# Performance work log

Measured on AMD Instinct MI355X. Metric: run time of the kernel, lower is better.

Reference implementation:

```python
import jax, jax.numpy as jnp
import numpy as np

D_MODEL, HEADS, D_K = 512, 8, 64
MIN_SPREAD, MIN_RBF, MAX_RBF = 2.0, 0.001, 1.0
NEG_INF = float('-inf')


def setup_inputs() -> dict:
    key = jax.random.key(0)
    ks = jax.random.split(key, 12)
    B, N = 2, 2048
    xav = (6.0 / (D_K + D_MODEL)) ** 0.5
    unif = lambda k, shape: jax.random.uniform(k, shape, jnp.float32, -xav, xav)
    return {
        'q': jax.random.normal(ks[0], (B, N, D_MODEL), jnp.float32),
        'k': jax.random.normal(ks[1], (B, N, D_MODEL), jnp.float32),
        'v': jax.random.normal(ks[2], (B, N, D_MODEL), jnp.float32),
        'coords': jax.random.normal(ks[3], (B, N, 3), jnp.float32),
        'mask': jnp.zeros((B, N), dtype=bool),
        'spread_weights': jnp.zeros((HEADS,), jnp.float32),
        'beta_weights': jnp.zeros((HEADS,), jnp.float32),
        'q_proj': unif(ks[4], (HEADS, D_MODEL, D_K)),
        'k_proj': unif(ks[5], (HEADS, D_MODEL, D_K)),
        'v_proj': unif(ks[6], (HEADS, D_MODEL, D_K)),
        'q_bias': jnp.zeros((HEADS, D_K), jnp.float32),
        'k_bias': jnp.zeros((HEADS, D_K), jnp.float32),
        'v_bias': jnp.zeros((HEADS, D_K), jnp.float32),
        'w_out': jax.random.normal(ks[7], (D_MODEL, D_MODEL), jnp.float32) * (1.0 / D_MODEL ** 0.5),
    }


def reference(q, k, v, coords, mask, spread_weights, beta_weights,
              q_proj, k_proj, v_proj, q_bias, k_bias, v_bias, w_out):
    B, N, _ = q.shape
    # per-head projections: [B,H,N,dk]
    Q = jnp.einsum('bnd,hdk->bhnk', q, q_proj) + q_bias[None, :, None, :]
    K = jnp.einsum('bnd,hdk->bhnk', k, k_proj) + k_bias[None, :, None, :]
    V = jnp.einsum('bnd,hdk->bhnk', v, v_proj) + v_bias[None, :, None, :]
    # scaled dot-product scores [B,H,N,N]
    S = jnp.einsum('bhnk,bhmk->bhnm', Q, K) / (D_K ** 0.5)
    # squared pairwise distances [B,N,N] (D = sqrt(D2); RBF uses -D^2 = -D2)
    D2 = jnp.sum((coords[:, :, None, :] - coords[:, None, :, :]) ** 2, axis=-1)
    spreads = MIN_SPREAD + jnp.exp(spread_weights)  # [H]
    betas = jnp.exp(beta_weights)                   # [H]
    R = jnp.exp(-D2[:, None, :, :] / (2.0 * spreads[None, :, None, None] ** 2))
    R_norm = 2.0 * (R - MIN_RBF) / (MAX_RBF - MIN_RBF) - 1.0
    SR = S + jnp.abs(S) * betas[None, :, None, None] * R_norm
    SR = jnp.where(mask[:, None, None, :], NEG_INF, SR)  # eval mode: drop_p = 0
    P = jax.nn.softmax(SR, axis=-1)
    out = jnp.einsum('bhnm,bhmk->bhnk', P, V)  # [B,H,N,dk]
    # permute(0,2,3,1) -> [B,N,dk,H], reshape to [B,N,d_model]
    out = jnp.transpose(out, (0, 2, 3, 1)).reshape(B, N, D_MODEL)
    return out @ w_out.T
```

## Files before the change

### kernel.cpp

```cpp
#include <hip/hip_runtime.h>
#include <hip/hip_fp16.h>

typedef unsigned short u16;
typedef unsigned int u32;
typedef __attribute__((ext_vector_type(4))) float f32x4;
typedef __attribute__((ext_vector_type(8))) short s16x8;
typedef __attribute__((ext_vector_type(2))) unsigned int u32x2;
typedef __fp16 fp16x2 __attribute__((ext_vector_type(2)));

#define B_SZ 2
#define N_SZ 2048
#define H_SZ 8
#define DK 64
#define DM 512
#define QSC 0.18033688f

static __device__ inline void mfma_f16(f32x4& acc, s16x8 a, s16x8 b) {
    asm volatile("v_mfma_f32_16x16x32_f16 %0, %1, %2, %0" : "+v"(acc) : "v"(a), "v"(b));
}
static __device__ inline u16 f16_rn(float f) { return __half_as_ushort(__float2half(f)); }

static __device__ inline u32 pkrtz(float a, float b) {
    union { fp16x2 h; u32 u; } cv;
    cv.h = __builtin_amdgcn_cvt_pkrtz(a, b);
    return cv.u;
}

#if __has_builtin(__builtin_amdgcn_exp2f)
#define EXP2(x) __builtin_amdgcn_exp2f(x)
#else
#define EXP2(x) exp2f(x)
#endif

static __device__ inline s16x8 cvt8(const float4& a, const float4& b) {
    s16x8 r;
    r[0] = (short)f16_rn(a.x); r[1] = (short)f16_rn(a.y);
    r[2] = (short)f16_rn(a.z); r[3] = (short)f16_rn(a.w);
    r[4] = (short)f16_rn(b.x); r[5] = (short)f16_rn(b.y);
    r[6] = (short)f16_rn(b.z); r[7] = (short)f16_rn(b.w);
    return r;
}

static __device__ inline u16* swz(u16* base, int row, int byteoff) {
    return (u16*)((char*)base + row * 128 + (byteoff ^ ((row & 7) << 4)));
}
static __device__ inline const u16* swzc(const u16* base, int row, int byteoff) {
    return (const u16*)((const char*)base + row * 128 + (byteoff ^ ((row & 7) << 4)));
}

#if __has_builtin(__builtin_amdgcn_global_load_lds)
#define HAS_GLL 1
static __device__ inline void gll16(const u16* g, u16* l) {
    __builtin_amdgcn_global_load_lds(
        (const __attribute__((address_space(1))) unsigned int*)g,
        (__attribute__((address_space(3))) unsigned int*)l, 16, 0, 0);
}
#endif
static __device__ inline void stage16(const u16* gp, u16* lbase, int lane) {
#ifdef HAS_GLL
    gll16(gp, lbase);
#else
    *(s16x8*)(lbase + lane * 8) = *(const s16x8*)(gp);
#endif
}

__global__ void __launch_bounds__(256) k_prep(
    const float* __restrict__ q, const float* __restrict__ k,
    const float* __restrict__ v, const float* __restrict__ qp,
    const float* __restrict__ kp, const float* __restrict__ vp,
    const float* __restrict__ wo, const float* __restrict__ coords,
    const unsigned char* __restrict__ maskp,
    u16* __restrict__ Pt, u16* __restrict__ Wb2, u16* __restrict__ Af,
    float4* __restrict__ C4, float* __restrict__ mbias) {
    int blk = blockIdx.x, t = threadIdx.x;
    __shared__ float lds[64 * 65];
    if (blk < 192) {
        int z = blk >> 6, rem = blk & 63, h = rem >> 3, ddt = rem & 7;
        const float* src = (z == 0 ? qp : (z == 1 ? kp : vp)) + (size_t)h * DM * DK;
        u16* dst = Pt + ((size_t)(z * H_SZ + h)) * DK * DM;
        float sc = (z == 0) ? QSC : 1.0f;
#pragma unroll
        for (int i = 0; i < 16; i++) {
            int idx = i * 256 + t;
            int rr = idx >> 6, cc = idx & 63;
            lds[cc * 65 + rr] = src[(size_t)(ddt * 64 + rr) * DK + cc];
        }
        __syncthreads();
#pragma unroll
        for (int i = 0; i < 16; i++) {
            int idx = i * 256 + t;
            int kk = idx >> 6, dd = idx & 63;
            dst[(size_t)kk * DM + ddt * 64 + dd] = f16_rn(lds[kk * 65 + dd] * sc);
        }
    } else if (blk < 320) {
        int idx8 = (blk - 192) * 256 + t;
        int base = idx8 * 8;
        int c = base >> 9, col0 = base & 511;
        int h = col0 >> 6, d0 = col0 & 63;
        s16x8 r;
#pragma unroll
        for (int i = 0; i < 8; i++)
            r[i] = (short)f16_rn(wo[(size_t)c * 512 + (d0 + i) * 8 + h]);
        *(s16x8*)(Wb2 + base) = r;
    } else if (blk < 3392) {
        size_t base = (size_t)(blk - 320) * 2048 + (size_t)t * 8;
        int z = (int)(base >> 21);
        size_t off = base & 2097151;
        const float* s = (z == 0 ? q : (z == 1 ? k : v)) + off;
        float4 f0 = *(const float4*)(s);
        float4 f1 = *(const float4*)(s + 4);
        *(s16x8*)(Af + base) = cvt8(f0, f1);
    } else {
        int i = (blk - 3392) * 256 + t;
        float x = coords[(size_t)i * 3], y = coords[(size_t)i * 3 + 1], z = coords[(size_t)i * 3 + 2];
        C4[i] = make_float4(x, y, z, x * x + y * y + z * z);
        mbias[i] = maskp[i] ? -1e30f : 0.0f;
    }
}

__global__ void __launch_bounds__(256) k_proj_gemm(
    const u16* __restrict__ Af, const u16* __restrict__ Pt,
    const float* __restrict__ qbias, const float* __restrict__ kbias,
    const float* __restrict__ vbias,
    u16* __restrict__ Qb, u16* __restrict__ Kb, u16* __restrict__ Vt) {
    int z = blockIdx.z;
    const u16* A = Af + (size_t)z * (4096 * 512);
    const float* bias = z == 0 ? qbias : (z == 1 ? kbias : vbias);
    const u16* Bw = Pt + (size_t)z * (512 * 512);
    int m0 = blockIdx.x * 128, c0 = blockIdx.y * 64;
    int t = threadIdx.x, w = t >> 6, l = t & 63, g = (l >> 4), cl = l & 15;
    __shared__ __align__(16) u16 a_lds[2][128 * 64];
    f32x4 acc[2][4] = {};
    int srow_b = w * 8 + (l >> 3), schk = l & 7;

#define STAGE_P(ks, buf)                                                              \
    {                                                                                 \
        _Pragma("unroll") for (int cc = 0; cc < 4; cc++) {                            \
            int row = cc * 32 + srow_b;                                               \
            const u16* gp = A + (size_t)(m0 + row) * 512 + (ks) * 64 +                \
                            ((schk ^ (row & 7)) << 3);                                \
            stage16(gp, a_lds[buf] + cc * 2048 + w * 512, l);                         \
        }                                                                             \
    }

    STAGE_P(0, 0);
    for (int ks = 0; ks < 8; ks++) {
        int cur = ks & 1;
        __syncthreads();
        if (ks < 7) STAGE_P(ks + 1, cur ^ 1);
        s16x8 bfrag[4][2];
#pragma unroll
        for (int st = 0; st < 4; st++) {
            int c = c0 + st * 16 + cl;
#pragma unroll
            for (int kk = 0; kk < 2; kk++)
                bfrag[st][kk] = *(const s16x8*)(Bw + (size_t)c * 512 + ks * 64 + kk * 32 + 8 * g);
        }
#pragma unroll
        for (int rs = 0; rs < 2; rs++) {
            int row = w * 32 + rs * 16 + cl;
#pragma unroll
            for (int kk = 0; kk < 2; kk++) {
                s16x8 afrag = *(const s16x8*)swzc(a_lds[cur], row, kk * 64 + 16 * g);
#pragma unroll
                for (int st = 0; st < 4; st++) mfma_f16(acc[rs][st], afrag, bfrag[st][kk]);
            }
        }
    }
#undef STAGE_P

    if (z == 2) {
        int h = blockIdx.y;
        int b = m0 >> 11;
        u16* vl = a_lds[0];
        __syncthreads();
#pragma unroll
        for (int rs = 0; rs < 2; rs++) {
#pragma unroll
            for (int st = 0; st < 4; st++) {
                int d = st * 16 + cl;
                float bv = bias[c0 + st * 16 + cl];
#pragma unroll
                for (int r = 0; r < 4; r++) {
                    int row = w * 32 + rs * 16 + 4 * g + r;
                    int jt = row >> 6, jl = row & 63;
                    int jp = (jl & 15) * 4 + (jl >> 4);
                    vl[jt * 4096 + d * 64 + jp] = f16_rn(acc[rs][st][r] + bv);
                }
            }
        }
        __syncthreads();
        int jt = t >> 7, rem = t & 127, d = rem >> 1, qh = t & 1;
        const u16* src = vl + jt * 4096 + d * 64 + qh * 32;
        int jtile = ((m0 & 2047) >> 6) + jt;
        u16* dst = Vt + ((size_t)((b * H_SZ + h) * 32 + jtile)) * 4096 + d * 64 + qh * 32;
        *(s16x8*)(dst) = *(const s16x8*)(src);
        *(s16x8*)(dst + 8) = *(const s16x8*)(src + 8);
        *(s16x8*)(dst + 16) = *(const s16x8*)(src + 16);
        *(s16x8*)(dst + 24) = *(const s16x8*)(src + 24);
    } else {
        float bsc = (z == 0) ? QSC : 1.0f;
        u16* dst = (z == 0) ? Qb : Kb;
#pragma unroll
        for (int rs = 0; rs < 2; rs++) {
#pragma unroll
            for (int st = 0; st < 4; st++) {
                int c = c0 + st * 16 + cl;
                int h = c >> 6, kk = c & 63;
                float bv = bias[c] * bsc;
#pragma unroll
                for (int r = 0; r < 4; r++) {
                    int m = m0 + w * 32 + rs * 16 + 4 * g + r;
                    int b = m >> 11, n = m & 2047;
                    dst[((size_t)(b * H_SZ + h) * N_SZ + n) * DK + kk] = f16_rn(acc[rs][st][r] + bv);
                }
            }
        }
    }
}

__global__ void __launch_bounds__(512, 4) k_attn(
    const u16* __restrict__ Qb, const u16* __restrict__ Kb,
    const u16* __restrict__ Vt, const float4* __restrict__ C4,
    const float* __restrict__ mbias,
    const float* __restrict__ spread_w, const float* __restrict__ beta_w,
    u16* __restrict__ Om) {
    int bid = blockIdx.x;
    int wid = (bid & 7) * 64 + (bid >> 3);
    int qt = wid & 31, bh = wid >> 5;
    int h = bh & 7, b = bh >> 3;
    int n0 = qt * 64;
    int t = threadIdx.x, w = t >> 6, l = t & 63, g = l >> 4, cl = l & 15;
    int wq = w & 3, half = w >> 2;

    __shared__ __align__(16) u16 kbuf[2][4096];
    __shared__ __align__(16) u16 vbuf[2][4096];
    __shared__ __align__(16) u16 pbuf[8][1024];
    __shared__ float4 cjs[2][64];
    __shared__ float mbs[2][64];

    int qrow = n0 + wq * 16 + cl;
    const u16* qp = Qb + ((size_t)bh * N_SZ + qrow) * DK;
    s16x8 qf0 = *(const s16x8*)(qp + 8 * g);
    s16x8 qf1 = *(const s16x8*)(qp + 32 + 8 * g);

    float sigma = 2.0f + __expf(spread_w[h]);
    float ninv2 = -0.72134752f / (sigma * sigma);
    float beta = __expf(beta_w[h]);
    float rnA = 2.002002f * beta, rnB = -1.002002f * beta;
    float m2n = -2.0f * ninv2;

    float qx2[4], qy2[4], qz2[4], aR[4];
#pragma unroll
    for (int r = 0; r < 4; r++) {
        float4 c4 = C4[b * N_SZ + n0 + wq * 16 + 4 * g + r];
        qx2[r] = c4.x * m2n; qy2[r] = c4.y * m2n; qz2[r] = c4.z * m2n;
        aR[r] = ninv2 * c4.w;
    }

    float mrun[4] = {-1e30f, -1e30f, -1e30f, -1e30f};
    float lsum[4] = {0.f, 0.f, 0.f, 0.f};
    f32x4 oacc[4] = {};

    int sid = t & 255, srow = sid >> 2, sq = sid & 3;
    const u16* kbase = Kb + (size_t)bh * N_SZ * DK;
    const u16* vbase = Vt + (size_t)bh * 32 * 4096;
    const float4* c4b = C4 + b * N_SZ;
    const float* mbb = mbias + b * N_SZ;

    s16x8 kst0, kst1, vst0, vst1;
    float4 cst; float mst = 0.f;

#define LOADT(it_)                                                                  \
    {                                                                               \
        int jts = (it_) * 2 + half, j0s = jts * 64;                                 \
        const u16* ksrc = kbase + (size_t)(j0s + srow) * 64 + sq * 16;              \
        kst0 = *(const s16x8*)(ksrc);                                               \
        kst1 = *(const s16x8*)(ksrc + 8);                                           \
        const u16* vsrc = vbase + (size_t)jts * 4096 + srow * 64 + sq * 16;         \
        vst0 = *(const s16x8*)(vsrc);                                               \
        vst1 = *(const s16x8*)(vsrc + 8);                                           \
        if (sid < 64) { cst = c4b[j0s + sid]; mst = mbb[j0s + sid]; }               \
    }

    LOADT(0);
    for (int it = 0; it < 16; it++) {
        __syncthreads();
        *(s16x8*)swz(kbuf[half], srow, sq * 32)      = kst0;
        *(s16x8*)swz(kbuf[half], srow, sq * 32 + 16) = kst1;
        *(s16x8*)swz(vbuf[half], srow, sq * 32)      = vst0;
        *(s16x8*)swz(vbuf[half], srow, sq * 32 + 16) = vst1;
        if (sid < 64) { cjs[half][sid] = cst; mbs[half][sid] = mst; }
        __syncthreads();
        if (it < 15) LOADT(it + 1);

        f32x4 s[4];
#pragma unroll
        for (int st = 0; st < 4; st++) {
            int jj = st * 16 + cl;
            s16x8 kf0 = *(const s16x8*)swzc(kbuf[half], jj, 16 * g);
            s16x8 kf1 = *(const s16x8*)swzc(kbuf[half], jj, 64 + 16 * g);
            f32x4 a = {};
            mfma_f16(a, qf0, kf0);
            mfma_f16(a, qf1, kf1);
            s[st] = a;
        }
        float sr[4][4];
#pragma unroll
        for (int st = 0; st < 4; st++) {
            float4 cc = cjs[half][st * 16 + cl];
            float mb = mbs[half][st * 16 + cl];
            float bJ = ninv2 * cc.w;
#pragma unroll
            for (int r = 0; r < 4; r++) {
                float arg = fmaf(qx2[r], cc.x,
                            fmaf(qy2[r], cc.y,
                            fmaf(qz2[r], cc.z, aR[r] + bJ)));
                float rb = EXP2(arg);
                float sv = s[st][r];
                sr[st][r] = fmaf(fabsf(sv), fmaf(rnA, rb, rnB), sv) + mb;
            }
        }
        float tmx[4]; bool need = false;
#pragma unroll
        for (int r = 0; r < 4; r++) {
            float tm = fmaxf(fmaxf(sr[0][r], sr[1][r]), fmaxf(sr[2][r], sr[3][r]));
            tm = fmaxf(tm, __shfl_xor(tm, 1));
            tm = fmaxf(tm, __shfl_xor(tm, 2));
            tm = fmaxf(tm, __shfl_xor(tm, 4));
            tm = fmaxf(tm, __shfl_xor(tm, 8));
            tmx[r] = tm;
            need = need || (tm > mrun[r] + 8.0f);
        }
        if (__any(need)) {
#pragma unroll
            for (int r = 0; r < 4; r++) {
                float mn = fmaxf(mrun[r], tmx[r]);
                float corr = EXP2(mrun[r] - mn);
                mrun[r] = mn;
                lsum[r] *= corr;
#pragma unroll
                for (int dst = 0; dst < 4; dst++) oacc[dst][r] *= corr;
            }
        }
#pragma unroll
        for (int r = 0; r < 4; r++) {
            float p0 = EXP2(sr[0][r] - mrun[r]);
            float p1 = EXP2(sr[1][r] - mrun[r]);
            float p2 = EXP2(sr[2][r] - mrun[r]);
            float p3 = EXP2(sr[3][r] - mrun[r]);
            lsum[r] += (p0 + p1) + (p2 + p3);
            u32x2 pw = {pkrtz(p0, p1), pkrtz(p2, p3)};
            *(u32x2*)swz(pbuf[w], 4 * g + r, cl * 8) = pw;
        }
#pragma unroll
        for (int ks = 0; ks < 2; ks++) {
            s16x8 pf = *(const s16x8*)swzc(pbuf[w], cl, ks * 64 + 16 * g);
#pragma unroll
            for (int dst = 0; dst < 4; dst++) {
                s16x8 vf = *(const s16x8*)swzc(vbuf[half], dst * 16 + cl, ks * 64 + 16 * g);
                mfma_f16(oacc[dst], pf, vf);
            }
        }
    }
#undef LOADT
#pragma unroll
    for (int r = 0; r < 4; r++) {
        float s = lsum[r];
        s += __shfl_xor(s, 1); s += __shfl_xor(s, 2);
        s += __shfl_xor(s, 4); s += __shfl_xor(s, 8);
        lsum[r] = s;
    }
    __syncthreads();
    float* scrO = (float*)(&kbuf[0][0]);
    float* scrM = (float*)(&vbuf[0][0]);
    if (half == 1) {
#pragma unroll
        for (int r = 0; r < 4; r++) {
            int rr = 4 * g + r;
#pragma unroll
            for (int dst = 0; dst < 4; dst++)
                scrO[wq * 1024 + rr * 64 + dst * 16 + cl] = oacc[dst][r];
            if (cl == 0) {
                scrM[wq * 32 + rr] = mrun[r];
                scrM[wq * 32 + 16 + rr] = lsum[r];
            }
        }
    }
    __syncthreads();
    if (half == 0) {
#pragma unroll
        for (int r = 0; r < 4; r++) {
            int rr = 4 * g + r;
            float mu = scrM[wq * 32 + rr], lu = scrM[wq * 32 + 16 + rr];
            float M = fmaxf(mrun[r], mu);
            float pa = EXP2(mrun[r] - M), pb = EXP2(mu - M);
            float inv = 1.0f / (pa * lsum[r] + pb * lu);
            int row = n0 + wq * 16 + rr;
#pragma unroll
            for (int dst = 0; dst < 4; dst++) {
                float o = (pa * oacc[dst][r] + pb * scrO[wq * 1024 + rr * 64 + dst * 16 + cl]) * inv;
                Om[((size_t)b * N_SZ + row) * DM + h * 64 + dst * 16 + cl] = f16_rn(o);
            }
        }
    }
}

__global__ void __launch_bounds__(256) k_out_gemm(
    const u16* __restrict__ Om, const u16* __restrict__ Wb2,
    float* __restrict__ out) {
    int m0 = blockIdx.x * 128, c0 = blockIdx.y * 64;
    int t = threadIdx.x, w = t >> 6, l = t & 63, g = (l >> 4), cl = l & 15;
    __shared__ __align__(16) u16 a_lds[2][128 * 64];
    f32x4 acc[2][4] = {};
    int srow_b = w * 8 + (l >> 3), schk = l & 7;

#define STAGE_O(ks, buf)                                                              \
    {                                                                                 \
        _Pragma("unroll") for (int cc = 0; cc < 4; cc++) {                            \
            int row = cc * 32 + srow_b;                                               \
            const u16* gp = Om + (size_t)(m0 + row) * 512 + (ks) * 64 +               \
                            ((schk ^ (row & 7)) << 3);                                \
            stage16(gp, a_lds[buf] + cc * 2048 + w * 512, l);                         \
        }                                                                             \
    }

    STAGE_O(0, 0);
    for (int ks = 0; ks < 8; ks++) {
        int cur = ks & 1;
        __syncthreads();
        if (ks < 7) STAGE_O(ks + 1, cur ^ 1);
        s16x8 bfrag[4][2];
#pragma unroll
        for (int st = 0; st < 4; st++) {
            int c = c0 + st * 16 + cl;
#pragma unroll
            for (int kk = 0; kk < 2; kk++)
                bfrag[st][kk] = *(const s16x8*)(Wb2 + (size_t)c * 512 + ks * 64 + kk * 32 + 8 * g);
        }
#pragma unroll
        for (int rs = 0; rs < 2; rs++) {
            int row = w * 32 + rs * 16 + cl;
#pragma unroll
            for (int kk = 0; kk < 2; kk++) {
                s16x8 afrag = *(const s16x8*)swzc(a_lds[cur], row, kk * 64 + 16 * g);
#pragma unroll
                for (int st = 0; st < 4; st++) mfma_f16(acc[rs][st], afrag, bfrag[st][kk]);
            }
        }
    }
#undef STAGE_O
#pragma unroll
    for (int rs = 0; rs < 2; rs++) {
#pragma unroll
        for (int st = 0; st < 4; st++) {
            int c = c0 + st * 16 + cl;
#pragma unroll
            for (int r = 0; r < 4; r++) {
                int m = m0 + w * 32 + rs * 16 + 4 * g + r;
                out[(size_t)m * 512 + c] = acc[rs][st][r];
            }
        }
    }
}

extern "C" void kernel_launch(void* const* d_in, const int* in_sizes, int n_in,
                              void* d_out, int out_size, void* d_ws, size_t ws_size,
                              hipStream_t stream) {
    const float* q      = (const float*)d_in[0];
    const float* k      = (const float*)d_in[1];
    const float* v      = (const float*)d_in[2];
    const float* coords = (const float*)d_in[3];
    const unsigned char* mask = (const unsigned char*)d_in[4];
    const float* sw     = (const float*)d_in[5];
    const float* bw     = (const float*)d_in[6];
    const float* qp     = (const float*)d_in[7];
    const float* kp     = (const float*)d_in[8];
    const float* vp     = (const float*)d_in[9];
    const float* qbias  = (const float*)d_in[10];
    const float* kbias  = (const float*)d_in[11];
    const float* vbias  = (const float*)d_in[12];
    const float* wo     = (const float*)d_in[13];

    char* ws = (char*)d_ws;
    u16*    Pt    = (u16*)(ws);
    u16*    Wb2   = (u16*)(ws + 1572864);
    u16*    Af    = (u16*)(ws + 2097152);
    u16*    Qb    = (u16*)(ws + 14680064);
    u16*    Kb    = (u16*)(ws + 18874368);
    u16*    Vt    = (u16*)(ws + 23068672);
    u16*    Om    = (u16*)(ws + 27262976);
    float4* C4    = (float4*)(ws + 31457280);
    float*  mbias = (float*)(ws + 31522816);

    k_prep<<<dim3(3408), 256, 0, stream>>>(q, k, v, qp, kp, vp, wo, coords, mask,
                                           Pt, Wb2, Af, C4, mbias);
    k_proj_gemm<<<dim3(32, 8, 3), 256, 0, stream>>>(Af, Pt, qbias, kbias, vbias, Qb, Kb, Vt);
    k_attn<<<dim3(512), 512, 0, stream>>>(Qb, Kb, Vt, C4, mbias, sw, bw, Om);
    k_out_gemm<<<dim3(32, 8), 256, 0, stream>>>(Om, Wb2, (float*)d_out);
}
```

Baseline: 240.5 us.

## Double-buffer attention K/V tiles via direct global-to-LDS loads and remap GEMM grids

The attention kernel now double-buffers K and V tiles in LDS, filling them with direct global-to-LDS loads (with XOR swizzle in the source address) instead of staging through registers. This removes one of the two barriers per iteration and lets the next tile's fetch overlap the current tile's compute. Per-key coords and mask values are now read straight from global memory rather than staged in LDS. The projection and output GEMMs switch to 1D grids with an XCD-aware block remap (bid&7 interleave), aimed at better L2 locality across the chiplets. LDS use in the attention kernel grows, which may reduce occupancy.

Result: faster. 203.0 us (-15.6%).

```diff
diff --git a/kernel.cpp b/kernel.cpp
--- a/kernel.cpp
+++ b/kernel.cpp
@@ -62,6 +62,21 @@
 #else
     *(s16x8*)(lbase + lane * 8) = *(const s16x8*)(gp);
 #endif
+}
+
+static __device__ inline void stage_tile_swz(const u16* tile, u16* lds, int wl, int lane) {
+#pragma unroll
+    for (int c = 0; c < 2; c++) {
+        int Lb = c * 4096 + wl * 1024 + lane * 16;
+        int row = Lb >> 7, off = Lb & 127;
+        const u16* src = tile + row * 64 + (((off ^ ((row & 7) << 4))) >> 1);
+        u16* dst = (u16*)((char*)lds + c * 4096 + wl * 1024);
+#ifdef HAS_GLL
+        gll16(src, dst);
+#else
+        *(s16x8*)((char*)dst + lane * 16) = *(const s16x8*)src;
+#endif
+    }
 }
 
 __global__ void __launch_bounds__(256) k_prep(
@@ -123,11 +138,15 @@
     const float* __restrict__ qbias, const float* __restrict__ kbias,
     const float* __restrict__ vbias,
     u16* __restrict__ Qb, u16* __restrict__ Kb, u16* __restrict__ Vt) {
-    int z = blockIdx.z;
+    int bid = blockIdx.x;
+    int wid = (bid & 7) * 96 + (bid >> 3);
+    int c0 = (wid & 7) * 64;
+    int zm = wid >> 3;
+    int m0 = (zm & 31) * 128;
+    int z = zm >> 5;
     const u16* A = Af + (size_t)z * (4096 * 512);
     const float* bias = z == 0 ? qbias : (z == 1 ? kbias : vbias);
     const u16* Bw = Pt + (size_t)z * (512 * 512);
-    int m0 = blockIdx.x * 128, c0 = blockIdx.y * 64;
     int t = threadIdx.x, w = t >> 6, l = t & 63, g = (l >> 4), cl = l & 15;
     __shared__ __align__(16) u16 a_lds[2][128 * 64];
     f32x4 acc[2][4] = {};
@@ -170,7 +189,7 @@
 #undef STAGE_P
 
     if (z == 2) {
-        int h = blockIdx.y;
+        int h = c0 >> 6;
         int b = m0 >> 11;
         u16* vl = a_lds[0];
         __syncthreads();
@@ -233,14 +252,11 @@
     int t = threadIdx.x, w = t >> 6, l = t & 63, g = l >> 4, cl = l & 15;
     int wq = w & 3, half = w >> 2;
 
-    __shared__ __align__(16) u16 kbuf[2][4096];
-    __shared__ __align__(16) u16 vbuf[2][4096];
+    __shared__ __align__(16) u16 kbuf[2][2][4096];
+    __shared__ __align__(16) u16 vbuf[2][2][4096];
     __shared__ __align__(16) u16 pbuf[8][1024];
-    __shared__ float4 cjs[2][64];
-    __shared__ float mbs[2][64];
-
-    int qrow = n0 + wq * 16 + cl;
-    const u16* qp = Qb + ((size_t)bh * N_SZ + qrow) * DK;
+
+    const u16* qp = Qb + ((size_t)bh * N_SZ + n0 + wq * 16 + cl) * DK;
     s16x8 qf0 = *(const s16x8*)(qp + 8 * g);
     s16x8 qf1 = *(const s16x8*)(qp + 32 + 8 * g);
 
@@ -262,44 +278,35 @@
     float lsum[4] = {0.f, 0.f, 0.f, 0.f};
     f32x4 oacc[4] = {};
 
-    int sid = t & 255, srow = sid >> 2, sq = sid & 3;
     const u16* kbase = Kb + (size_t)bh * N_SZ * DK;
     const u16* vbase = Vt + (size_t)bh * 32 * 4096;
     const float4* c4b = C4 + b * N_SZ;
     const float* mbb = mbias + b * N_SZ;
 
-    s16x8 kst0, kst1, vst0, vst1;
-    float4 cst; float mst = 0.f;
-
-#define LOADT(it_)                                                                  \
-    {                                                                               \
-        int jts = (it_) * 2 + half, j0s = jts * 64;                                 \
-        const u16* ksrc = kbase + (size_t)(j0s + srow) * 64 + sq * 16;              \
-        kst0 = *(const s16x8*)(ksrc);                                               \
-        kst1 = *(const s16x8*)(ksrc + 8);                                           \
-        const u16* vsrc = vbase + (size_t)jts * 4096 + srow * 64 + sq * 16;         \
-        vst0 = *(const s16x8*)(vsrc);                                               \
-        vst1 = *(const s16x8*)(vsrc + 8);                                           \
-        if (sid < 64) { cst = c4b[j0s + sid]; mst = mbb[j0s + sid]; }               \
-    }
-
-    LOADT(0);
+    stage_tile_swz(kbase + (size_t)(half * 64) * 64, &kbuf[0][half][0], wq, l);
+    stage_tile_swz(vbase + (size_t)half * 4096,      &vbuf[0][half][0], wq, l);
+
     for (int it = 0; it < 16; it++) {
+        int cur = it & 1;
+        int jt = it * 2 + half, j0 = jt * 64;
         __syncthreads();
-        *(s16x8*)swz(kbuf[half], srow, sq * 32)      = kst0;
-        *(s16x8*)swz(kbuf[half], srow, sq * 32 + 16) = kst1;
-        *(s16x8*)swz(vbuf[half], srow, sq * 32)      = vst0;
-        *(s16x8*)swz(vbuf[half], srow, sq * 32 + 16) = vst1;
-        if (sid < 64) { cjs[half][sid] = cst; mbs[half][sid] = mst; }
-        __syncthreads();
-        if (it < 15) LOADT(it + 1);
-
+        if (it < 15) {
+            int jn = jt + 2;
+            stage_tile_swz(kbase + (size_t)(jn * 64) * 64, &kbuf[cur ^ 1][half][0], wq, l);
+            stage_tile_swz(vbase + (size_t)jn * 4096,      &vbuf[cur ^ 1][half][0], wq, l);
+        }
+        float4 ccv[4]; float mbv[4];
+#pragma unroll
+        for (int st = 0; st < 4; st++) {
+            ccv[st] = c4b[j0 + st * 16 + cl];
+            mbv[st] = mbb[j0 + st * 16 + cl];
+        }
         f32x4 s[4];
 #pragma unroll
         for (int st = 0; st < 4; st++) {
             int jj = st * 16 + cl;
-            s16x8 kf0 = *(const s16x8*)swzc(kbuf[half], jj, 16 * g);
-            s16x8 kf1 = *(const s16x8*)swzc(kbuf[half], jj, 64 + 16 * g);
+            s16x8 kf0 = *(const s16x8*)swzc(&kbuf[cur][half][0], jj, 16 * g);
+            s16x8 kf1 = *(const s16x8*)swzc(&kbuf[cur][half][0], jj, 64 + 16 * g);
             f32x4 a = {};
             mfma_f16(a, qf0, kf0);
             mfma_f16(a, qf1, kf1);
@@ -308,17 +315,15 @@
         float sr[4][4];
 #pragma unroll
         for (int st = 0; st < 4; st++) {
-            float4 cc = cjs[half][st * 16 + cl];
-            float mb = mbs[half][st * 16 + cl];
-            float bJ = ninv2 * cc.w;
+            float bJ = ninv2 * ccv[st].w;
 #pragma unroll
             for (int r = 0; r < 4; r++) {
-                float arg = fmaf(qx2[r], cc.x,
-                            fmaf(qy2[r], cc.y,
-                            fmaf(qz2[r], cc.z, aR[r] + bJ)));
+                float arg = fmaf(qx2[r], ccv[st].x,
+                            fmaf(qy2[r], ccv[st].y,
+                            fmaf(qz2[r], ccv[st].z, aR[r] + bJ)));
                 float rb = EXP2(arg);
                 float sv = s[st][r];
-                sr[st][r] = fmaf(fabsf(sv), fmaf(rnA, rb, rnB), sv) + mb;
+                sr[st][r] = fmaf(fabsf(sv), fmaf(rnA, rb, rnB), sv) + mbv[st];
             }
         }
         float tmx[4]; bool need = false;
@@ -358,12 +363,11 @@
             s16x8 pf = *(const s16x8*)swzc(pbuf[w], cl, ks * 64 + 16 * g);
 #pragma unroll
             for (int dst = 0; dst < 4; dst++) {
-                s16x8 vf = *(const s16x8*)swzc(vbuf[half], dst * 16 + cl, ks * 64 + 16 * g);
+                s16x8 vf = *(const s16x8*)swzc(&vbuf[cur][half][0], dst * 16 + cl, ks * 64 + 16 * g);
                 mfma_f16(oacc[dst], pf, vf);
             }
         }
     }
-#undef LOADT
 #pragma unroll
     for (int r = 0; r < 4; r++) {
         float s = lsum[r];
@@ -372,8 +376,8 @@
         lsum[r] = s;
     }
     __syncthreads();
-    float* scrO = (float*)(&kbuf[0][0]);
-    float* scrM = (float*)(&vbuf[0][0]);
+    float* scrO = (float*)(&kbuf[0][0][0]);
+    float* scrM = (float*)(&vbuf[0][0][0]);
     if (half == 1) {
 #pragma unroll
         for (int r = 0; r < 4; r++) {
@@ -409,7 +413,10 @@
 __global__ void __launch_bounds__(256) k_out_gemm(
     const u16* __restrict__ Om, const u16* __restrict__ Wb2,
     float* __restrict__ out) {
-    int m0 = blockIdx.x * 128, c0 = blockIdx.y * 64;
+    int bid = blockIdx.x;
+    int wid = (bid & 7) * 32 + (bid >> 3);
+    int c0 = (wid & 7) * 64;
+    int m0 = (wid >> 3) * 128;
     int t = threadIdx.x, w = t >> 6, l = t & 63, g = (l >> 4), cl = l & 15;
     __shared__ __align__(16) u16 a_lds[2][128 * 64];
     f32x4 acc[2][4] = {};
@@ -495,7 +502,7 @@
 
     k_prep<<<dim3(3408), 256, 0, stream>>>(q, k, v, qp, kp, vp, wo, coords, mask,
                                            Pt, Wb2, Af, C4, mbias);
-    k_proj_gemm<<<dim3(32, 8, 3), 256, 0, stream>>>(Af, Pt, qbias, kbias, vbias, Qb, Kb, Vt);
+    k_proj_gemm<<<dim3(768), 256, 0, stream>>>(Af, Pt, qbias, kbias, vbias, Qb, Kb, Vt);
     k_attn<<<dim3(512), 512, 0, stream>>>(Qb, Kb, Vt, C4, mbias, sw, bw, Om);
-    k_out_gemm<<<dim3(32, 8), 256, 0, stream>>>(Om, Wb2, (float*)d_out);
-}
+    k_out_gemm<<<dim3(256), 256, 0, stream>>>(Om, Wb2, (float*)d_out);
+}
```
